# Kernel optimization log

Measured on AMD Instinct MI355X. Metric: run time of the kernel, lower is better.

## Reference

```python
import jax, jax.numpy as jnp
import numpy as np

L, D, H, NP, PS, C, OUT, N = 8, 768, 12, 14, 16, 3, 1000, 32
DH = D // H
S = NP * NP + 1  # 197 tokens (cls + patches)
EPS = 1e-5


def pos_embeddings(seq_len, d):
    # result[i,j] = sin(i/10000^(j/d)) if j even else cos(i/10000^((j-1)/d))
    i = np.arange(seq_len)[:, None].astype(np.float64)
    j = np.arange(d)[None, :]
    ang = i / (10000.0 ** ((j - (j % 2)) / d))
    pe = np.where(j % 2 == 0, np.sin(ang), np.cos(ang))
    return jnp.asarray(pe, dtype=jnp.float32)


def setup_inputs() -> dict:
    key = jax.random.key(0)
    ks = jax.random.split(key, 16)
    s = 0.02
    return {
        'images': jax.random.normal(ks[0], (N, C, NP * PS, NP * PS), jnp.float32),
        'Wm': jax.random.normal(ks[1], (C * PS * PS, D), jnp.float32) * s,
        'bm': jnp.zeros((D,), jnp.float32),
        'cls_tok': jax.random.uniform(ks[2], (1, D), jnp.float32),
        'pos_emb': pos_embeddings(S, D),
        'ln1_w': jnp.ones((L, D), jnp.float32),
        'ln1_b': jnp.zeros((L, D), jnp.float32),
        'Wq': jax.random.normal(ks[3], (L, H, DH, DH), jnp.float32) * s,
        'bq': jnp.zeros((L, H, DH), jnp.float32),
        'Wk': jax.random.normal(ks[4], (L, H, DH, DH), jnp.float32) * s,
        'bk': jnp.zeros((L, H, DH), jnp.float32),
        'Wv': jax.random.normal(ks[5], (L, H, DH, DH), jnp.float32) * s,
        'bv': jnp.zeros((L, H, DH), jnp.float32),
        'ln2_w': jnp.ones((L, D), jnp.float32),
        'ln2_b': jnp.zeros((L, D), jnp.float32),
        'W1': jax.random.normal(ks[6], (L, D, 4 * D), jnp.float32) * s,
        'b1': jnp.zeros((L, 4 * D), jnp.float32),
        'W2': jax.random.normal(ks[7], (L, 4 * D, D), jnp.float32) * s,
        'b2': jnp.zeros((L, D), jnp.float32),
        'Wout': jax.random.normal(ks[8], (D, OUT), jnp.float32) * s,
        'bout': jnp.zeros((OUT,), jnp.float32),
    }


def layernorm(x, w, b):
    mu = x.mean(-1, keepdims=True)
    var = ((x - mu) ** 2).mean(-1, keepdims=True)
    return (x - mu) * jax.lax.rsqrt(var + EPS) * w + b


def vit_forward(images, Wm, bm, cls_tok, pos_emb, ln1_w, ln1_b, Wq, bq, Wk, bk, Wv, bv,
                ln2_w, ln2_b, W1, b1, W2, b2, Wout, bout):
    n = images.shape[0]
    # patchify: (n,c,h,w) -> (n, NP*NP, C*PS*PS), each patch flattened in (c,ph,pw) order
    patches = images.reshape(n, C, NP, PS, NP, PS).transpose(0, 2, 4, 1, 3, 5)
    patches = patches.reshape(n, NP * NP, C * PS * PS)
    tokens = patches @ Wm + bm                                   # [n, S-1, D]
    tokens = jnp.concatenate([jnp.broadcast_to(cls_tok, (n, 1, D)), tokens], axis=1)
    out = tokens + pos_emb                                       # [n, S, D]

    scale = 1.0 / jnp.sqrt(jnp.asarray(DH, jnp.float32))

    def block(x, p):
        l1w, l1b, wq, bq_, wk, bk_, wv, bv_, l2w, l2b, w1, b1_, w2, b2_ = p
        h = layernorm(x, l1w, l1b).reshape(n, S, H, DH)
        q = jnp.einsum('nshd,hde->nshe', h, wq) + bq_
        k = jnp.einsum('nshd,hde->nshe', h, wk) + bk_
        v = jnp.einsum('nshd,hde->nshe', h, wv) + bv_
        att = jax.nn.softmax(jnp.einsum('nshe,nthe->nhst', q, k) * scale, axis=-1)
        o = jnp.einsum('nhst,nthe->nshe', att, v).reshape(n, S, D)
        x = x + o
        h2 = layernorm(x, l2w, l2b)
        x = x + (jax.nn.gelu(h2 @ w1 + b1_, approximate=False) @ w2 + b2_)
        return x, None

    out, _ = jax.lax.scan(block, out, (ln1_w, ln1_b, Wq, bq, Wk, bk, Wv, bv,
                                       ln2_w, ln2_b, W1, b1, W2, b2))
    cls = out[:, 0]                                              # [n, D]
    return jax.nn.softmax(cls @ Wout + bout, axis=-1)            # [n, OUT]


def reference(images, Wm, bm, cls_tok, pos_emb, ln1_w, ln1_b, Wq, bq, Wk, bk, Wv, bv,
              ln2_w, ln2_b, W1, b1, W2, b2, Wout, bout):
    return vit_forward(images, Wm, bm, cls_tok, pos_emb, ln1_w, ln1_b, Wq, bq, Wk, bk,
                       Wv, bv, ln2_w, ln2_b, W1, b1, W2, b2, Wout, bout)
```

## Files before the change

kernel.cpp:

```cpp
#include <hip/hip_runtime.h>
#include <math.h>

#define N_ 32
#define S_ 197
#define D_ 768
#define H_ 12
#define L_ 8
#define FF_ 3072
#define MTOK (N_ * S_)
#define ND (N_ * S_ * D_)

typedef __attribute__((ext_vector_type(8))) short short8x;
typedef __attribute__((ext_vector_type(4))) float floatx4;
typedef unsigned short ushort_t;
typedef unsigned int uint_t;

__device__ __forceinline__ ushort_t f2bf_rn(float x) {
  uint_t u = __float_as_uint(x);
  uint_t r = (u + 0x7fff + ((u >> 16) & 1)) >> 16;
  return (ushort_t)r;
}
__device__ __forceinline__ float bf2f(ushort_t h) {
  return __uint_as_float(((uint_t)h) << 16);
}

__global__ __launch_bounds__(256) void patchify_kernel(const float* __restrict__ img,
                                                       ushort_t* __restrict__ phi,
                                                       ushort_t* __restrict__ plo) {
  int idx = blockIdx.x * 256 + threadIdx.x;
  if (idx >= 6272 * 768) return;
  int mp = idx / 768, kk = idx - mp * 768;
  int n = mp / 196, p = mp - n * 196;
  int py = p / 14, px = p - py * 14;
  int c = kk >> 8, r = kk & 255;
  int u = r >> 4, vv = r & 15;
  float val = img[((size_t)(n * 3 + c) * 224 + py * 16 + u) * 224 + px * 16 + vv];
  ushort_t hi = f2bf_rn(val);
  phi[idx] = hi;
  plo[idx] = f2bf_rn(val - bf2f(hi));
}

__global__ __launch_bounds__(256) void cls_init_kernel(const float* __restrict__ cls_tok,
                                                       const float* __restrict__ pos,
                                                       float* __restrict__ x) {
  int idx = blockIdx.x * 256 + threadIdx.x;
  int n = idx / 768, d = idx - n * 768;
  x[(size_t)n * S_ * D_ + d] = cls_tok[d] + pos[d];
}

__global__ __launch_bounds__(256) void wconvert_kernel(const float* __restrict__ W,
                                                       ushort_t* __restrict__ Thi,
                                                       ushort_t* __restrict__ Tlo, int K, int N) {
  __shared__ float T[32][36];
  int n0 = blockIdx.x * 32, k0 = blockIdx.y * 32;
  int t = threadIdx.x;
  int r = t >> 3, c4 = (t & 7) * 4;
  float4 v = *(const float4*)&W[(size_t)(k0 + r) * N + n0 + c4];
  T[c4 + 0][r] = v.x;
  T[c4 + 1][r] = v.y;
  T[c4 + 2][r] = v.z;
  T[c4 + 3][r] = v.w;
  __syncthreads();
  ushort4 hi, lo;
  float a;
  a = T[r][c4 + 0]; hi.x = f2bf_rn(a); lo.x = f2bf_rn(a - bf2f(hi.x));
  a = T[r][c4 + 1]; hi.y = f2bf_rn(a); lo.y = f2bf_rn(a - bf2f(hi.y));
  a = T[r][c4 + 2]; hi.z = f2bf_rn(a); lo.z = f2bf_rn(a - bf2f(hi.z));
  a = T[r][c4 + 3]; hi.w = f2bf_rn(a); lo.w = f2bf_rn(a - bf2f(hi.w));
  size_t o = (size_t)(n0 + r) * K + k0 + c4;
  *(ushort4*)&Thi[o] = hi;
  *(ushort4*)&Tlo[o] = lo;
}

#define EPI_PATCH 1
#define EPI_GELU 2
#define EPI_RES 3
#define LDST 40

template <int EPI>
__global__ __launch_bounds__(256) void gemm_mfma(
    const ushort_t* __restrict__ Ahi, const ushort_t* __restrict__ Alo,
    const ushort_t* __restrict__ Bhi, const ushort_t* __restrict__ Blo,
    const float* __restrict__ bias, float* __restrict__ Cf, ushort_t* __restrict__ Chi,
    ushort_t* __restrict__ Clo, int M, int K, int Nc, const float* __restrict__ pos) {
  __shared__ ushort_t As[2][128 * LDST];
  __shared__ ushort_t Bs[2][128 * LDST];
  int tid = threadIdx.x;
  int wave = tid >> 6, lane = tid & 63;
  int wr = (wave >> 1) * 64, wc = (wave & 1) * 64;
  int q = lane >> 4, l15 = lane & 15;
  int m0 = blockIdx.y * 128, n0 = blockIdx.x * 128;

  floatx4 acc[4][4];
#pragma unroll
  for (int i = 0; i < 4; ++i)
#pragma unroll
    for (int j = 0; j < 4; ++j)
#pragma unroll
      for (int e = 0; e < 4; ++e) acc[i][j][e] = 0.f;

  int sr = tid >> 2;
  int kq = tid & 3;

  for (int k0 = 0; k0 < K; k0 += 32) {
#pragma unroll
    for (int it = 0; it < 2; ++it) {
      int rr = it * 64 + sr;
      int gm = m0 + rr;
      if (gm > M - 1) gm = M - 1;
      size_t aoff = (size_t)gm * K + k0 + kq * 8;
      *(uint4*)&As[0][rr * LDST + kq * 8] = *(const uint4*)&Ahi[aoff];
      *(uint4*)&As[1][rr * LDST + kq * 8] = *(const uint4*)&Alo[aoff];
      size_t boff = (size_t)(n0 + rr) * K + k0 + kq * 8;
      *(uint4*)&Bs[0][rr * LDST + kq * 8] = *(const uint4*)&Bhi[boff];
      *(uint4*)&Bs[1][rr * LDST + kq * 8] = *(const uint4*)&Blo[boff];
    }
    __syncthreads();
    short8x ah[4], al[4], bh[4], bl[4];
    int abase = (wr + l15) * LDST + q * 8;
    int bbase = (wc + l15) * LDST + q * 8;
#pragma unroll
    for (int i = 0; i < 4; ++i) {
      ah[i] = *(const short8x*)&As[0][abase + i * 16 * LDST];
      al[i] = *(const short8x*)&As[1][abase + i * 16 * LDST];
      bh[i] = *(const short8x*)&Bs[0][bbase + i * 16 * LDST];
      bl[i] = *(const short8x*)&Bs[1][bbase + i * 16 * LDST];
    }
#pragma unroll
    for (int i = 0; i < 4; ++i)
#pragma unroll
      for (int j = 0; j < 4; ++j) {
        acc[i][j] = __builtin_amdgcn_mfma_f32_16x16x32_bf16(ah[i], bh[j], acc[i][j], 0, 0, 0);
        acc[i][j] = __builtin_amdgcn_mfma_f32_16x16x32_bf16(ah[i], bl[j], acc[i][j], 0, 0, 0);
        acc[i][j] = __builtin_amdgcn_mfma_f32_16x16x32_bf16(al[i], bh[j], acc[i][j], 0, 0, 0);
      }
    __syncthreads();
  }

#pragma unroll
  for (int i = 0; i < 4; ++i) {
#pragma unroll
    for (int j = 0; j < 4; ++j) {
      int col = n0 + wc + j * 16 + l15;
#pragma unroll
      for (int r4 = 0; r4 < 4; ++r4) {
        int gr = m0 + wr + i * 16 + q * 4 + r4;
        if (gr >= M) continue;
        float v = acc[i][j][r4] + bias[col];
        if (EPI == EPI_PATCH) {
          int n = gr / 196, t = gr - n * 196 + 1;
          Cf[((size_t)n * S_ + t) * 768 + col] = v + pos[(size_t)t * 768 + col];
        } else if (EPI == EPI_GELU) {
          float g = 0.5f * v * (1.f + erff(v * 0.70710678118654752f));
          ushort_t hi = f2bf_rn(g);
          size_t o = (size_t)gr * FF_ + col;
          Chi[o] = hi;
          Clo[o] = f2bf_rn(g - bf2f(hi));
        } else {
          Cf[(size_t)gr * 768 + col] += v;
        }
      }
    }
  }
}

__global__ __launch_bounds__(256) void ln_kernel(const float* __restrict__ x,
                                                 ushort_t* __restrict__ hhi,
                                                 ushort_t* __restrict__ hlo,
                                                 const float* __restrict__ w,
                                                 const float* __restrict__ b) {
  int tok = blockIdx.x * 4 + (threadIdx.x >> 6);
  int lane = threadIdx.x & 63;
  const float* xr = x + (size_t)tok * 768;
  float4 v[3];
  float s = 0.f, s2 = 0.f;
#pragma unroll
  for (int i = 0; i < 3; ++i) {
    v[i] = *(const float4*)&xr[i * 256 + lane * 4];
    s += v[i].x + v[i].y + v[i].z + v[i].w;
    s2 += v[i].x * v[i].x + v[i].y * v[i].y + v[i].z * v[i].z + v[i].w * v[i].w;
  }
#pragma unroll
  for (int m = 32; m > 0; m >>= 1) { s += __shfl_xor(s, m, 64); s2 += __shfl_xor(s2, m, 64); }
  float mu = s * (1.f / 768.f);
  float var = s2 * (1.f / 768.f) - mu * mu;
  float rs = rsqrtf(var + 1e-5f);
#pragma unroll
  for (int i = 0; i < 3; ++i) {
    float4 wv = *(const float4*)&w[i * 256 + lane * 4];
    float4 bv = *(const float4*)&b[i * 256 + lane * 4];
    float o0 = (v[i].x - mu) * rs * wv.x + bv.x;
    float o1 = (v[i].y - mu) * rs * wv.y + bv.y;
    float o2 = (v[i].z - mu) * rs * wv.z + bv.z;
    float o3 = (v[i].w - mu) * rs * wv.w + bv.w;
    ushort4 oh, ol;
    oh.x = f2bf_rn(o0); ol.x = f2bf_rn(o0 - bf2f(oh.x));
    oh.y = f2bf_rn(o1); ol.y = f2bf_rn(o1 - bf2f(oh.y));
    oh.z = f2bf_rn(o2); ol.z = f2bf_rn(o2 - bf2f(oh.z));
    oh.w = f2bf_rn(o3); ol.w = f2bf_rn(o3 - bf2f(oh.w));
    size_t o = (size_t)tok * 768 + i * 256 + lane * 4;
    *(ushort4*)&hhi[o] = oh;
    *(ushort4*)&hlo[o] = ol;
  }
}

#define KSTR 72

__global__ __launch_bounds__(256) void qkv_mfma(
    const ushort_t* __restrict__ hhi, const ushort_t* __restrict__ hlo,
    const float* __restrict__ Wq, const float* __restrict__ Wk, const float* __restrict__ Wv,
    const float* __restrict__ bq, const float* __restrict__ bk, const float* __restrict__ bv,
    ushort_t* __restrict__ qhi, ushort_t* __restrict__ qlo, ushort_t* __restrict__ khi,
    ushort_t* __restrict__ klo, ushort_t* __restrict__ vhi, ushort_t* __restrict__ vlo) {
  __shared__ ushort_t As[2][128 * KSTR];
  __shared__ ushort_t Ws[2][64 * KSTR];
  int tid = threadIdx.x;
  int wave = tid >> 6, lane = tid & 63;
  int q = lane >> 4, l15 = lane & 15;
  int m0 = blockIdx.x * 128, h = blockIdx.y;
  int wm = wave >> 1, wj = wave & 1;

#pragma unroll
  for (int p = 0; p < 2; ++p) {
    const ushort_t* src = p == 0 ? hhi : hlo;
#pragma unroll
    for (int it = 0; it < 4; ++it) {
      int idx = it * 256 + tid;
      int r = idx >> 3, c = idx & 7;
      int gm = m0 + r;
      if (gm > MTOK - 1) gm = MTOK - 1;
      *(uint4*)&As[p][r * KSTR + c * 8] = *(const uint4*)&src[(size_t)gm * 768 + h * 64 + c * 8];
    }
  }

  const float* Wmat[3] = {Wq + (size_t)h * 4096, Wk + (size_t)h * 4096, Wv + (size_t)h * 4096};
  const float* Bmat[3] = {bq + h * 64, bk + h * 64, bv + h * 64};
  ushort_t* Ohi[3] = {qhi, khi, vhi};
  ushort_t* Olo[3] = {qlo, klo, vlo};

  for (int mat = 0; mat < 3; ++mat) {
    __syncthreads();
#pragma unroll
    for (int it = 0; it < 4; ++it) {
      int idx = it * 256 + tid;
      int r = idx >> 4, c4 = (idx & 15) * 4;
      float4 wv = *(const float4*)&Wmat[mat][r * 64 + c4];
      float vals[4] = {wv.x, wv.y, wv.z, wv.w};
#pragma unroll
      for (int i = 0; i < 4; ++i) {
        ushort_t hi = f2bf_rn(vals[i]);
        Ws[0][(c4 + i) * KSTR + r] = hi;
        Ws[1][(c4 + i) * KSTR + r] = f2bf_rn(vals[i] - bf2f(hi));
      }
    }
    __syncthreads();

    floatx4 acc[4][2];
#pragma unroll
    for (int i = 0; i < 4; ++i)
#pragma unroll
      for (int j = 0; j < 2; ++j)
#pragma unroll
        for (int e = 0; e < 4; ++e) acc[i][j][e] = 0.f;

#pragma unroll
    for (int ks = 0; ks < 2; ++ks) {
      short8x bh[2], bl[2];
#pragma unroll
      for (int j = 0; j < 2; ++j) {
        int bb = (wj * 32 + j * 16 + l15) * KSTR + ks * 32 + q * 8;
        bh[j] = *(const short8x*)&Ws[0][bb];
        bl[j] = *(const short8x*)&Ws[1][bb];
      }
#pragma unroll
      for (int i = 0; i < 4; ++i) {
        int ab = (wm * 64 + i * 16 + l15) * KSTR + ks * 32 + q * 8;
        short8x ah = *(const short8x*)&As[0][ab];
        short8x al = *(const short8x*)&As[1][ab];
#pragma unroll
        for (int j = 0; j < 2; ++j) {
          acc[i][j] = __builtin_amdgcn_mfma_f32_16x16x32_bf16(ah, bh[j], acc[i][j], 0, 0, 0);
          acc[i][j] = __builtin_amdgcn_mfma_f32_16x16x32_bf16(ah, bl[j], acc[i][j], 0, 0, 0);
          acc[i][j] = __builtin_amdgcn_mfma_f32_16x16x32_bf16(al, bh[j], acc[i][j], 0, 0, 0);
        }
      }
    }
#pragma unroll
    for (int i = 0; i < 4; ++i)
#pragma unroll
      for (int j = 0; j < 2; ++j) {
        int col = wj * 32 + j * 16 + l15;
        float bias = Bmat[mat][col];
#pragma unroll
        for (int r = 0; r < 4; ++r) {
          int tok = m0 + wm * 64 + i * 16 + q * 4 + r;
          if (tok >= MTOK) continue;
          float v = acc[i][j][r] + bias;
          ushort_t hi = f2bf_rn(v);
          size_t o = (size_t)tok * 768 + h * 64 + col;
          Ohi[mat][o] = hi;
          Olo[mat][o] = f2bf_rn(v - bf2f(hi));
        }
      }
  }
}

__global__ __launch_bounds__(256) void attn_mfma(
    const ushort_t* __restrict__ qhi, const ushort_t* __restrict__ qlo,
    const ushort_t* __restrict__ khi, const ushort_t* __restrict__ klo,
    const ushort_t* __restrict__ vhi, const ushort_t* __restrict__ vlo,
    float* __restrict__ X) {
  __shared__ ushort_t Qs[2][64 * KSTR];
  __shared__ ushort_t Ks[2][64 * KSTR];
  __shared__ ushort_t Vs[2][64 * KSTR];
  int tid = threadIdx.x;
  int wave = tid >> 6, lane = tid & 63;
  int q = lane >> 4, l15 = lane & 15;
  int qc = blockIdx.x, h = blockIdx.y, n = blockIdx.z;
  int q0 = qc * 64;
  int row0 = wave * 16;

#pragma unroll
  for (int p = 0; p < 2; ++p) {
    const ushort_t* src = p == 0 ? qhi : qlo;
#pragma unroll
    for (int it = 0; it < 2; ++it) {
      int idx = it * 256 + tid;
      int r = idx >> 3, c = idx & 7;
      int gr = q0 + r;
      if (gr > S_ - 1) gr = S_ - 1;
      *(uint4*)&Qs[p][r * KSTR + c * 8] =
          *(const uint4*)&src[((size_t)n * S_ + gr) * 768 + h * 64 + c * 8];
    }
  }
  __syncthreads();
  short8x qa_h[2], qa_l[2];
#pragma unroll
  for (int ks = 0; ks < 2; ++ks) {
    int ab = (row0 + l15) * KSTR + ks * 32 + q * 8;
    qa_h[ks] = *(const short8x*)&Qs[0][ab];
    qa_l[ks] = *(const short8x*)&Qs[1][ab];
  }

  float mrow[4], lrow[4];
  floatx4 oa[4];
#pragma unroll
  for (int r = 0; r < 4; ++r) { mrow[r] = -INFINITY; lrow[r] = 0.f; }
#pragma unroll
  for (int j = 0; j < 4; ++j)
#pragma unroll
    for (int e = 0; e < 4; ++e) oa[j][e] = 0.f;

  for (int t = 0; t < 4; ++t) {
    __syncthreads();
#pragma unroll
    for (int p = 0; p < 2; ++p) {
      const ushort_t* src = p == 0 ? khi : klo;
#pragma unroll
      for (int it = 0; it < 2; ++it) {
        int idx = it * 256 + tid;
        int r = idx >> 3, c = idx & 7;
        int gk = t * 64 + r;
        if (gk > S_ - 1) gk = S_ - 1;
        *(uint4*)&Ks[p][r * KSTR + c * 8] =
            *(const uint4*)&src[((size_t)n * S_ + gk) * 768 + h * 64 + c * 8];
      }
    }
    {
      int d = tid & 63, kg = tid >> 6;
#pragma unroll
      for (int p = 0; p < 2; ++p) {
        const ushort_t* src = p == 0 ? vhi : vlo;
#pragma unroll
        for (int k4 = 0; k4 < 4; ++k4) {
          ushort4 pk;
          ushort_t tmp[4];
#pragma unroll
          for (int i = 0; i < 4; ++i) {
            int gk = t * 64 + kg * 16 + k4 * 4 + i;
            if (gk > S_ - 1) gk = S_ - 1;
            tmp[i] = src[((size_t)n * S_ + gk) * 768 + h * 64 + d];
          }
          pk.x = tmp[0]; pk.y = tmp[1]; pk.z = tmp[2]; pk.w = tmp[3];
          *(ushort4*)&Vs[p][d * KSTR + kg * 16 + k4 * 4] = pk;
        }
      }
    }
    __syncthreads();

    floatx4 sc[4];
#pragma unroll
    for (int j = 0; j < 4; ++j) {
#pragma unroll
      for (int e = 0; e < 4; ++e) sc[j][e] = 0.f;
#pragma unroll
      for (int ks = 0; ks < 2; ++ks) {
        int bb = (j * 16 + l15) * KSTR + ks * 32 + q * 8;
        short8x kb_h = *(const short8x*)&Ks[0][bb];
        short8x kb_l = *(const short8x*)&Ks[1][bb];
        sc[j] = __builtin_amdgcn_mfma_f32_16x16x32_bf16(qa_h[ks], kb_h, sc[j], 0, 0, 0);
        sc[j] = __builtin_amdgcn_mfma_f32_16x16x32_bf16(qa_h[ks], kb_l, sc[j], 0, 0, 0);
        sc[j] = __builtin_amdgcn_mfma_f32_16x16x32_bf16(qa_l[ks], kb_h, sc[j], 0, 0, 0);
      }
    }
    __syncthreads();

    bool kvalid[4];
#pragma unroll
    for (int j = 0; j < 4; ++j) kvalid[j] = (t * 64 + j * 16 + l15) < S_;
#pragma unroll
    for (int r = 0; r < 4; ++r) {
      float sv[4];
#pragma unroll
      for (int j = 0; j < 4; ++j) sv[j] = kvalid[j] ? sc[j][r] * 0.125f : -INFINITY;
      float mx = fmaxf(fmaxf(sv[0], sv[1]), fmaxf(sv[2], sv[3]));
#pragma unroll
      for (int msk = 1; msk < 16; msk <<= 1) mx = fmaxf(mx, __shfl_xor(mx, msk, 64));
      float mn = fmaxf(mrow[r], mx);
      float al = expf(mrow[r] - mn);
      float p[4], ps = 0.f;
#pragma unroll
      for (int j = 0; j < 4; ++j) { p[j] = expf(sv[j] - mn); ps += p[j]; }
#pragma unroll
      for (int msk = 1; msk < 16; msk <<= 1) ps += __shfl_xor(ps, msk, 64);
      lrow[r] = lrow[r] * al + ps;
      mrow[r] = mn;
#pragma unroll
      for (int j = 0; j < 4; ++j) oa[j][r] *= al;
      int prow = (row0 + q * 4 + r) * KSTR;
#pragma unroll
      for (int j = 0; j < 4; ++j) {
        ushort_t phv = f2bf_rn(p[j]);
        Ks[0][prow + j * 16 + l15] = phv;
        Ks[1][prow + j * 16 + l15] = f2bf_rn(p[j] - bf2f(phv));
      }
    }

#pragma unroll
    for (int ks = 0; ks < 2; ++ks) {
      int ab = (row0 + l15) * KSTR + ks * 32 + q * 8;
      short8x pa_h = *(const short8x*)&Ks[0][ab];
      short8x pa_l = *(const short8x*)&Ks[1][ab];
#pragma unroll
      for (int j = 0; j < 4; ++j) {
        int bb = (j * 16 + l15) * KSTR + ks * 32 + q * 8;
        short8x vb_h = *(const short8x*)&Vs[0][bb];
        short8x vb_l = *(const short8x*)&Vs[1][bb];
        oa[j] = __builtin_amdgcn_mfma_f32_16x16x32_bf16(pa_h, vb_h, oa[j], 0, 0, 0);
        oa[j] = __builtin_amdgcn_mfma_f32_16x16x32_bf16(pa_h, vb_l, oa[j], 0, 0, 0);
        oa[j] = __builtin_amdgcn_mfma_f32_16x16x32_bf16(pa_l, vb_h, oa[j], 0, 0, 0);
      }
    }
  }

#pragma unroll
  for (int r = 0; r < 4; ++r) {
    int row = q0 + row0 + q * 4 + r;
    if (row >= S_) continue;
    float invl = 1.f / lrow[r];
#pragma unroll
    for (int j = 0; j < 4; ++j)
      X[((size_t)n * S_ + row) * 768 + h * 64 + j * 16 + l15] += oa[j][r] * invl;
  }
}

__global__ __launch_bounds__(256) void head_kernel(const float* __restrict__ x,
                                                   const float* __restrict__ Wout,
                                                   const float* __restrict__ bout,
                                                   float* __restrict__ out) {
  __shared__ float cls[768];
  __shared__ float red[4];
  int n = blockIdx.x, tid = threadIdx.x;
  int w = tid >> 6, lane = tid & 63;
  for (int d = tid; d < 768; d += 256) cls[d] = x[(size_t)n * S_ * D_ + d];
  __syncthreads();
  int j0 = tid * 4;
  bool act = j0 < 1000;
  float a0 = 0.f, a1 = 0.f, a2 = 0.f, a3 = 0.f;
  if (act) {
    for (int kk = 0; kk < 768; ++kk) {
      float c = cls[kk];
      float4 wv = *(const float4*)&Wout[(size_t)kk * 1000 + j0];
      a0 += c * wv.x;
      a1 += c * wv.y;
      a2 += c * wv.z;
      a3 += c * wv.w;
    }
    a0 += bout[j0];
    a1 += bout[j0 + 1];
    a2 += bout[j0 + 2];
    a3 += bout[j0 + 3];
  }
  float mx = act ? fmaxf(fmaxf(a0, a1), fmaxf(a2, a3)) : -INFINITY;
#pragma unroll
  for (int m = 32; m > 0; m >>= 1) mx = fmaxf(mx, __shfl_xor(mx, m, 64));
  if (lane == 0) red[w] = mx;
  __syncthreads();
  mx = fmaxf(fmaxf(red[0], red[1]), fmaxf(red[2], red[3]));
  __syncthreads();
  float e0 = 0.f, e1 = 0.f, e2 = 0.f, e3 = 0.f, ss = 0.f;
  if (act) {
    e0 = expf(a0 - mx);
    e1 = expf(a1 - mx);
    e2 = expf(a2 - mx);
    e3 = expf(a3 - mx);
    ss = e0 + e1 + e2 + e3;
  }
#pragma unroll
  for (int m = 32; m > 0; m >>= 1) ss += __shfl_xor(ss, m, 64);
  if (lane == 0) red[w] = ss;
  __syncthreads();
  ss = red[0] + red[1] + red[2] + red[3];
  if (act) {
    float inv = 1.f / ss;
    out[(size_t)n * 1000 + j0] = e0 * inv;
    out[(size_t)n * 1000 + j0 + 1] = e1 * inv;
    out[(size_t)n * 1000 + j0 + 2] = e2 * inv;
    out[(size_t)n * 1000 + j0 + 3] = e3 * inv;
  }
}

extern "C" void kernel_launch(void* const* d_in, const int* in_sizes, int n_in, void* d_out,
                              int out_size, void* d_ws, size_t ws_size, hipStream_t stream) {
  const float* images = (const float*)d_in[0];
  const float* Wm = (const float*)d_in[1];
  const float* bm = (const float*)d_in[2];
  const float* cls_tok = (const float*)d_in[3];
  const float* pos_emb = (const float*)d_in[4];
  const float* ln1_w = (const float*)d_in[5];
  const float* ln1_b = (const float*)d_in[6];
  const float* Wq = (const float*)d_in[7];
  const float* bq = (const float*)d_in[8];
  const float* Wk = (const float*)d_in[9];
  const float* bk = (const float*)d_in[10];
  const float* Wv = (const float*)d_in[11];
  const float* bv = (const float*)d_in[12];
  const float* ln2_w = (const float*)d_in[13];
  const float* ln2_b = (const float*)d_in[14];
  const float* W1 = (const float*)d_in[15];
  const float* b1 = (const float*)d_in[16];
  const float* W2 = (const float*)d_in[17];
  const float* b2 = (const float*)d_in[18];
  const float* Wout = (const float*)d_in[19];
  const float* bout = (const float*)d_in[20];
  float* out = (float*)d_out;

  char* base = (char*)d_ws;
  float* x = (float*)base;
  ushort_t* hhi = (ushort_t*)(base + (size_t)ND * 4);
  ushort_t* hlo = hhi + (size_t)ND;
  char* R = base + (size_t)ND * 8;
  ushort_t* qhi = (ushort_t*)R;
  ushort_t* qlo = qhi + (size_t)ND;
  ushort_t* khi = qlo + (size_t)ND;
  ushort_t* klo = khi + (size_t)ND;
  ushort_t* vhi = klo + (size_t)ND;
  ushort_t* vlo = vhi + (size_t)ND;
  ushort_t* ghi = (ushort_t*)R;
  ushort_t* glo = ghi + (size_t)MTOK * FF_;
  ushort_t* phi = (ushort_t*)R;
  ushort_t* plo = phi + (size_t)6272 * 768;
  char* WB = R + (size_t)MTOK * FF_ * 4;
  ushort_t* w1hi = (ushort_t*)WB;
  ushort_t* w1lo = w1hi + (size_t)768 * FF_;
  ushort_t* w2hi = w1lo + (size_t)768 * FF_;
  ushort_t* w2lo = w2hi + (size_t)768 * FF_;

  patchify_kernel<<<(6272 * 768 + 255) / 256, 256, 0, stream>>>(images, phi, plo);
  wconvert_kernel<<<dim3(24, 24), 256, 0, stream>>>(Wm, w1hi, w1lo, 768, 768);
  gemm_mfma<EPI_PATCH><<<dim3(6, 49), 256, 0, stream>>>(phi, plo, w1hi, w1lo, bm, x, nullptr,
                                                        nullptr, 6272, 768, 768, pos_emb);
  cls_init_kernel<<<(32 * 768) / 256, 256, 0, stream>>>(cls_tok, pos_emb, x);

  for (int l = 0; l < 8; ++l) {
    ln_kernel<<<MTOK / 4, 256, 0, stream>>>(x, hhi, hlo, ln1_w + l * 768, ln1_b + l * 768);
    qkv_mfma<<<dim3(50, 12), 256, 0, stream>>>(
        hhi, hlo, Wq + (size_t)l * 49152, Wk + (size_t)l * 49152, Wv + (size_t)l * 49152,
        bq + l * 768, bk + l * 768, bv + l * 768, qhi, qlo, khi, klo, vhi, vlo);
    attn_mfma<<<dim3(4, 12, 32), 256, 0, stream>>>(qhi, qlo, khi, klo, vhi, vlo, x);
    ln_kernel<<<MTOK / 4, 256, 0, stream>>>(x, hhi, hlo, ln2_w + l * 768, ln2_b + l * 768);
    wconvert_kernel<<<dim3(96, 24), 256, 0, stream>>>(W1 + (size_t)l * 768 * FF_, w1hi, w1lo,
                                                      768, FF_);
    gemm_mfma<EPI_GELU><<<dim3(24, 50), 256, 0, stream>>>(hhi, hlo, w1hi, w1lo, b1 + l * FF_,
                                                          nullptr, ghi, glo, MTOK, 768, FF_,
                                                          nullptr);
    wconvert_kernel<<<dim3(24, 96), 256, 0, stream>>>(W2 + (size_t)l * FF_ * 768, w2hi, w2lo,
                                                      FF_, 768);
    gemm_mfma<EPI_RES><<<dim3(6, 50), 256, 0, stream>>>(ghi, glo, w2hi, w2lo, b2 + l * 768, x,
                                                        nullptr, nullptr, MTOK, FF_, 768,
                                                        nullptr);
  }
  head_kernel<<<32, 256, 0, stream>>>(x, Wout, bout, out);
}
```

Before: 3.970 ms.

## Split-K the FFN down-projection GEMM with atomic residual accumulation

The W2 GEMM (K=3072, only 300 tiles) now splits K in two across blockIdx.z and accumulates into the residual stream with atomic float adds. Only the first split adds the bias. The grid mapping is also swapped so blockIdx.x walks M tiles, which changes which tiles run together and share weight columns in cache. More tiles fill the GPU better, at the cost of atomic traffic and a result that can vary slightly from run to run.

```diff
diff --git a/kernel.cpp b/kernel.cpp
--- a/kernel.cpp
+++ b/kernel.cpp
@@ -74,10 +74,10 @@
 
 #define EPI_PATCH 1
 #define EPI_GELU 2
-#define EPI_RES 3
+#define EPI_ATOM 3
 #define LDST 40
 
-template <int EPI>
+template <int EPI, int KP>
 __global__ __launch_bounds__(256) void gemm_mfma(
     const ushort_t* __restrict__ Ahi, const ushort_t* __restrict__ Alo,
     const ushort_t* __restrict__ Bhi, const ushort_t* __restrict__ Blo,
@@ -89,7 +89,9 @@
   int wave = tid >> 6, lane = tid & 63;
   int wr = (wave >> 1) * 64, wc = (wave & 1) * 64;
   int q = lane >> 4, l15 = lane & 15;
-  int m0 = blockIdx.y * 128, n0 = blockIdx.x * 128;
+  int m0 = blockIdx.x * 128, n0 = blockIdx.y * 128;
+  int kbeg = (KP > 1) ? blockIdx.z * (K / KP) : 0;
+  int kend = kbeg + K / KP;
 
   floatx4 acc[4][4];
 #pragma unroll
@@ -102,7 +104,7 @@
   int sr = tid >> 2;
   int kq = tid & 3;
 
-  for (int k0 = 0; k0 < K; k0 += 32) {
+  for (int k0 = kbeg; k0 < kend; k0 += 32) {
 #pragma unroll
     for (int it = 0; it < 2; ++it) {
       int rr = it * 64 + sr;
@@ -146,18 +148,22 @@
       for (int r4 = 0; r4 < 4; ++r4) {
         int gr = m0 + wr + i * 16 + q * 4 + r4;
         if (gr >= M) continue;
-        float v = acc[i][j][r4] + bias[col];
-        if (EPI == EPI_PATCH) {
-          int n = gr / 196, t = gr - n * 196 + 1;
-          Cf[((size_t)n * S_ + t) * 768 + col] = v + pos[(size_t)t * 768 + col];
-        } else if (EPI == EPI_GELU) {
-          float g = 0.5f * v * (1.f + erff(v * 0.70710678118654752f));
-          ushort_t hi = f2bf_rn(g);
-          size_t o = (size_t)gr * FF_ + col;
-          Chi[o] = hi;
-          Clo[o] = f2bf_rn(g - bf2f(hi));
+        if (EPI == EPI_ATOM) {
+          float v = acc[i][j][r4];
+          if (KP == 1 || blockIdx.z == 0) v += bias[col];
+          unsafeAtomicAdd(&Cf[(size_t)gr * 768 + col], v);
         } else {
-          Cf[(size_t)gr * 768 + col] += v;
+          float v = acc[i][j][r4] + bias[col];
+          if (EPI == EPI_PATCH) {
+            int n = gr / 196, t = gr - n * 196 + 1;
+            Cf[((size_t)n * S_ + t) * 768 + col] = v + pos[(size_t)t * 768 + col];
+          } else {
+            float g = 0.5f * v * (1.f + erff(v * 0.70710678118654752f));
+            ushort_t hi = f2bf_rn(g);
+            size_t o = (size_t)gr * FF_ + col;
+            Chi[o] = hi;
+            Clo[o] = f2bf_rn(g - bf2f(hi));
+          }
         }
       }
     }
@@ -568,8 +574,9 @@
 
   patchify_kernel<<<(6272 * 768 + 255) / 256, 256, 0, stream>>>(images, phi, plo);
   wconvert_kernel<<<dim3(24, 24), 256, 0, stream>>>(Wm, w1hi, w1lo, 768, 768);
-  gemm_mfma<EPI_PATCH><<<dim3(6, 49), 256, 0, stream>>>(phi, plo, w1hi, w1lo, bm, x, nullptr,
-                                                        nullptr, 6272, 768, 768, pos_emb);
+  gemm_mfma<EPI_PATCH, 1><<<dim3(49, 6), 256, 0, stream>>>(phi, plo, w1hi, w1lo, bm, x,
+                                                           nullptr, nullptr, 6272, 768, 768,
+                                                           pos_emb);
   cls_init_kernel<<<(32 * 768) / 256, 256, 0, stream>>>(cls_tok, pos_emb, x);
 
   for (int l = 0; l < 8; ++l) {
@@ -581,14 +588,15 @@
     ln_kernel<<<MTOK / 4, 256, 0, stream>>>(x, hhi, hlo, ln2_w + l * 768, ln2_b + l * 768);
     wconvert_kernel<<<dim3(96, 24), 256, 0, stream>>>(W1 + (size_t)l * 768 * FF_, w1hi, w1lo,
                                                       768, FF_);
-    gemm_mfma<EPI_GELU><<<dim3(24, 50), 256, 0, stream>>>(hhi, hlo, w1hi, w1lo, b1 + l * FF_,
-                                                          nullptr, ghi, glo, MTOK, 768, FF_,
-                                                          nullptr);
+    gemm_mfma<EPI_GELU, 1><<<dim3(50, 24), 256, 0, stream>>>(hhi, hlo, w1hi, w1lo, b1 + l * FF_,
+                                                             nullptr, ghi, glo, MTOK, 768, FF_,
+                                                             nullptr);
     wconvert_kernel<<<dim3(24, 96), 256, 0, stream>>>(W2 + (size_t)l * FF_ * 768, w2hi, w2lo,
                                                       FF_, 768);
-    gemm_mfma<EPI_RES><<<dim3(6, 50), 256, 0, stream>>>(ghi, glo, w2hi, w2lo, b2 + l * 768, x,
-                                                        nullptr, nullptr, MTOK, FF_, 768,
-                                                        nullptr);
+    gemm_mfma<EPI_ATOM, 2><<<dim3(50, 6, 2), 256, 0, stream>>>(ghi, glo, w2hi, w2lo,
+                                                               b2 + l * 768, x, nullptr,
+                                                               nullptr, MTOK, FF_, 768,
+                                                               nullptr);
   }
   head_kernel<<<32, 256, 0, stream>>>(x, Wout, bout, out);
 }
```

Result: no change. 3.927 ms (-1.1%).
